# Kernel optimization log

Hardware: AMD Instinct MI355X
Metric: run time of the kernel (lower is better)

The kernel has to match this reference:

```python
import jax, jax.numpy as jnp
import numpy as np

D = 1024      # features
C = 768       # context dim
H = 16        # heads
HD = D // H   # head dim = 64
N = 2048      # query tokens
M = 2048      # context tokens
EPS = 1e-12
SCALE = float(np.sqrt(HD))


def layernorm(x, w, b):
    c = x - x.mean(axis=-1, keepdims=True)
    s = (c * c).mean(axis=-1, keepdims=True)
    return c * jax.lax.rsqrt(s + EPS) * w + b


def setup_inputs() -> dict:
    key = jax.random.key(0)
    ks = jax.random.split(key, 10)
    sc = 0.02
    return {
        "x": jax.random.normal(ks[0], (N, D), jnp.float32),
        "ctx": jax.random.normal(ks[1], (M, C), jnp.float32),
        # attention projections (Projection: normal*0.02, zero bias)
        "wq": jax.random.normal(ks[2], (D, D), jnp.float32) * sc,
        "bq": jnp.zeros((D,), jnp.float32),
        "wk": jax.random.normal(ks[3], (C, D), jnp.float32) * sc,
        "bk": jnp.zeros((D,), jnp.float32),
        "wv": jax.random.normal(ks[4], (C, D), jnp.float32) * sc,
        "bv": jnp.zeros((D,), jnp.float32),
        "wo": jax.random.normal(ks[5], (D, D), jnp.float32) * sc,
        "bo": jnp.zeros((D,), jnp.float32),
        # MLP
        "w1": jax.random.normal(ks[6], (D, 4 * D), jnp.float32) * sc,
        "b1": jnp.zeros((4 * D,), jnp.float32),
        "w2": jax.random.normal(ks[7], (4 * D, D), jnp.float32) * sc,
        "b2": jnp.zeros((D,), jnp.float32),
        # layernorms
        "qn_w": jnp.ones((D,), jnp.float32), "qn_b": jnp.zeros((D,), jnp.float32),
        "kvn_w": jnp.ones((C,), jnp.float32), "kvn_b": jnp.zeros((C,), jnp.float32),
        "pn_w": jnp.ones((D,), jnp.float32), "pn_b": jnp.zeros((D,), jnp.float32),
    }


def reference(x, ctx, wq, bq, wk, bk, wv, bv, wo, bo, w1, b1, w2, b2,
              qn_w, qn_b, kvn_w, kvn_b, pn_w, pn_b):
    # pre-norm cross-attention
    xq = layernorm(x, qn_w, qn_b)          # [n, d]
    kv = layernorm(ctx, kvn_w, kvn_b)      # [m, c]
    q = (xq @ wq + bq).reshape(N, H, HD).transpose(1, 0, 2)   # [h, n, hd]
    k = (kv @ wk + bk).reshape(M, H, HD).transpose(1, 0, 2)   # [h, m, hd]
    v = (kv @ wv + bv).reshape(M, H, HD).transpose(1, 0, 2)   # [h, m, hd]
    attn = jax.nn.softmax(jnp.einsum('hnd,hmd->hnm', q, k) / SCALE, axis=-1)
    o = jnp.einsum('hnm,hmd->hnd', attn, v).transpose(1, 0, 2).reshape(N, D)
    x = (o @ wo + bo) + x
    # MLP block
    h = layernorm(x, pn_w, pn_b)
    h = jax.nn.gelu(h @ w1 + b1) @ w2 + b2
    return h + x
```

## Files before the change

### kernel.cpp

```cpp
#include <hip/hip_runtime.h>

typedef __bf16 bf16;
typedef __bf16 bf16x4 __attribute__((ext_vector_type(4)));
typedef __bf16 bf16x8 __attribute__((ext_vector_type(8)));
typedef float f32x4 __attribute__((ext_vector_type(4)));

#define N_TOK 2048
#define M_TOK 2048
#define DIM 1024
#define CDIM 768
#define DFF 4096

static __device__ __forceinline__ void async16(const void* g, void* l) {
  __builtin_amdgcn_global_load_lds((const __attribute__((address_space(1))) void*)g,
                                   (__attribute__((address_space(3))) void*)l, 16, 0, 0);
}

__device__ __forceinline__ bool detect_bf(const void* xprobe, float* sbuf) {
  int* cnt = (int*)sbuf;
  if (threadIdx.x == 0) *cnt = 0;
  __syncthreads();
  const unsigned* w = (const unsigned*)xprobe;
  int ok = 0;
  for (int i = threadIdx.x; i < 512; i += 256) {
    unsigned lo = w[i] & 0xFFFFu;
    float f = __uint_as_float(lo << 16);
    if (lo == 0u || (fabsf(f) > 1e-3f && fabsf(f) < 1e3f)) ok++;
  }
  atomicAdd(cnt, ok);
  __syncthreads();
  return *cnt >= 256;
}

__device__ __forceinline__ void t32(int bx, int by, const void* in, bf16* out,
                                    int r0, int Rcnt, int c0, int Cfull,
                                    bool isbf, bf16* t) {
  const int cb = bx * 32, rb = by * 32;
  const int tx = threadIdx.x & 31, ty = threadIdx.x >> 5;
#pragma unroll
  for (int i = 0; i < 4; i++) {
    const size_t r = (size_t)(r0 + rb + ty + i * 8);
    const size_t c = (size_t)(c0 + cb + tx);
    float v = isbf ? (float)((const bf16*)in)[r * Cfull + c]
                   : ((const float*)in)[r * Cfull + c];
    t[(ty + i * 8) * 33 + tx] = (bf16)v;
  }
  __syncthreads();
#pragma unroll
  for (int i = 0; i < 4; i++)
    out[(size_t)(cb + ty + i * 8) * Rcnt + rb + tx] = t[tx * 33 + ty + i * 8];
}

__device__ __forceinline__ void ln_row(const void* x, const void* wr, const void* br,
                                       bf16* outp, int cols, int row,
                                       bool in_bf, bool w_bf,
                                       float* xrow, float* sh) {
  const bf16* xr_b = (const bf16*)x + (size_t)row * cols;
  const float* xr_f = (const float*)x + (size_t)row * cols;
  bf16* orow = outp + (size_t)row * cols;
  float s = 0.f, ss = 0.f;
  for (int c = threadIdx.x; c < cols; c += 256) {
    float v = in_bf ? (float)xr_b[c] : xr_f[c];
    xrow[c] = v;
    s += v; ss += v * v;
  }
  for (int d = 1; d < 64; d <<= 1) { s += __shfl_xor(s, d, 64); ss += __shfl_xor(ss, d, 64); }
  const int wv = threadIdx.x >> 6, lane = threadIdx.x & 63;
  if (lane == 0) { sh[wv] = s; sh[4 + wv] = ss; }
  __syncthreads();
  s = sh[0] + sh[1] + sh[2] + sh[3];
  ss = sh[4] + sh[5] + sh[6] + sh[7];
  const float mean = s / cols;
  float var = ss / cols - mean * mean;
  var = fmaxf(var, 0.f);
  const float r = rsqrtf(var + 1e-12f);
  for (int c = threadIdx.x; c < cols; c += 256) {
    const float wv2 = w_bf ? (float)((const bf16*)wr)[c] : ((const float*)wr)[c];
    const float bv2 = w_bf ? (float)((const bf16*)br)[c] : ((const float*)br)[c];
    orow[c] = (bf16)((xrow[c] - mean) * r * wv2 + bv2);
  }
}

struct PrepArgs {
  const void* tsrc[4]; bf16* tdst[4]; int tRcnt[4], tCfull[4], tgy[4];
  const void* x; const void* qnw; const void* qnb; bf16* xq;
  const void* ctx; const void* kvnw; const void* kvnb; bf16* kvn;
  const void* csrc[12]; bf16* cdst[12]; int cn[12];
  const void* xprobe;
};
__global__ __launch_bounds__(256) void prep_kernel(PrepArgs a, int* flag) {
  __shared__ __align__(16) float sbuf[1040];
  const int z = blockIdx.z;
  const bool isbf = detect_bf(a.xprobe, sbuf);
  if (z < 4) {
    if ((int)blockIdx.y >= a.tgy[z]) return;
    t32(blockIdx.x, blockIdx.y, a.tsrc[z], a.tdst[z], 0, a.tRcnt[z], 0, a.tCfull[z],
        isbf, (bf16*)sbuf);
  } else if (z < 8) {
    const int row = blockIdx.x + 32 * blockIdx.y + (z & 1) * 1024;
    if (z < 6) ln_row(a.x,   a.qnw,  a.qnb,  a.xq,  DIM,  row, isbf, isbf, sbuf, sbuf + 1024);
    else       ln_row(a.ctx, a.kvnw, a.kvnb, a.kvn, CDIM, row, isbf, isbf, sbuf, sbuf + 1024);
  } else {
    const int b = blockIdx.x + 32 * blockIdx.y;
    if (b == 0 && threadIdx.x == 0) *flag = isbf ? 1 : 0;
    if (b >= 12) return;
    const void* in = a.csrc[b];
    bf16* out = a.cdst[b];
    const int n = a.cn[b];
    for (int i = threadIdx.x; i < n; i += 256)
      out[i] = isbf ? ((const bf16*)in)[i] : (bf16)((const float*)in)[i];
  }
}

struct PostArgs {
  const void* w1; bf16* w1T;
  const void* w2; bf16* w2T;
  const bf16* xat; const void* pnw; const void* pnb; bf16* hln;
};
__global__ __launch_bounds__(256) void post_kernel(PostArgs a, const int* flag) {
  __shared__ __align__(16) float sbuf[1040];
  const int z = blockIdx.z;
  const bool isbf = (*flag != 0);
  if (z == 0) {
    t32(blockIdx.x, blockIdx.y, a.w1, a.w1T, 0, DIM, 0, DFF, isbf, (bf16*)sbuf);
  } else if (z == 1) {
    const int tbx = blockIdx.x & 31, tby = blockIdx.y + 32 * (blockIdx.x >> 5);
    t32(tbx, tby, a.w2, a.w2T, 0, 2048, 0, DIM, isbf, (bf16*)sbuf);
  } else {
    const int row = blockIdx.x + 64 * blockIdx.y;
    ln_row(a.xat, a.pnw, a.pnb, a.hln, DIM, row, true, isbf, sbuf, sbuf + 1024);
  }
}

__device__ __forceinline__ float gelu_f(float x) {
  float u = 0.7978845608028654f * (x + 0.044715f * x * x * x);
  return 0.5f * x * (1.f + tanhf(u));
}

template <int EPI>
__device__ __forceinline__ void gemm_body(
    int bx, int by,
    const bf16* __restrict__ A, const bf16* __restrict__ Bt,
    const bf16* __restrict__ bias, const void* __restrict__ resid,
    void* __restrict__ Cout, int K, int ldc, const int* flag) {
  __shared__ __align__(16) bf16 As[2][64 * 64];
  __shared__ __align__(16) bf16 Bs[2][64 * 64];
  const int tid = threadIdx.x;
  const int lane = tid & 63, wv = tid >> 6;
  const int lq = lane >> 4, lm = lane & 15;
  const int row0 = by * 64, col0 = bx * 64;
  const int wr = (wv >> 1) * 32, wc = (wv & 1) * 32;

  const int sr = lane >> 3;
  const int sc = ((lane & 7) ^ sr) * 8;
  const int swz = (lm & 7) << 3;

  f32x4 acc[2][2] = {};

  const bf16* Abase = A + (size_t)(row0 + wv * 16 + sr) * K + sc;
  const bf16* Bbase = Bt + (size_t)(col0 + wv * 16 + sr) * K + sc;

  const int nt = K >> 6;
#pragma unroll
  for (int b = 0; b < 2; b++) {
    async16(Abase + (size_t)(b * 8) * K, &As[0][wv * 1024 + b * 512]);
    async16(Bbase + (size_t)(b * 8) * K, &Bs[0][wv * 1024 + b * 512]);
  }
  __syncthreads();

  int cur = 0;
  for (int t = 0; t < nt; ++t) {
    if (t + 1 < nt) {
      const int k1 = (t + 1) << 6;
#pragma unroll
      for (int b = 0; b < 2; b++) {
        async16(Abase + (size_t)(b * 8) * K + k1, &As[cur ^ 1][wv * 1024 + b * 512]);
        async16(Bbase + (size_t)(b * 8) * K + k1, &Bs[cur ^ 1][wv * 1024 + b * 512]);
      }
    }
#pragma unroll
    for (int kh = 0; kh < 2; kh++) {
      const int cofs = (kh * 32 + lq * 8) ^ swz;
      bf16x8 af[2], bfv[2];
#pragma unroll
      for (int i = 0; i < 2; i++)
        af[i] = *(const bf16x8*)&As[cur][(wr + i * 16 + lm) * 64 + cofs];
#pragma unroll
      for (int j = 0; j < 2; j++)
        bfv[j] = *(const bf16x8*)&Bs[cur][(wc + j * 16 + lm) * 64 + cofs];
#pragma unroll
      for (int i = 0; i < 2; i++)
#pragma unroll
        for (int j = 0; j < 2; j++)
          acc[i][j] = __builtin_amdgcn_mfma_f32_16x16x32_bf16(af[i], bfv[j], acc[i][j], 0, 0, 0);
    }
    __syncthreads();
    cur ^= 1;
  }

  const bool isbf = (*flag != 0);
#pragma unroll
  for (int i = 0; i < 2; i++) {
    const int rb = row0 + wr + i * 16 + lq * 4;
#pragma unroll
    for (int j = 0; j < 2; j++) {
      const int c = col0 + wc + j * 16 + lm;
      const float bv = (EPI != 5) ? (float)bias[c] : 0.f;
#pragma unroll
      for (int rg = 0; rg < 4; rg++) {
        const size_t idx = (size_t)(rb + rg) * ldc + c;
        float v = acc[i][j][rg] + bv;
        if (EPI == 1)
          v += isbf ? (float)((const bf16*)resid)[idx] : ((const float*)resid)[idx];
        if (EPI == 2) v = gelu_f(v);
        if (EPI == 4) v += (float)((const bf16*)resid)[idx];
        if (EPI == 5)
          v += isbf ? (float)((bf16*)Cout)[idx] : ((float*)Cout)[idx];
        if (EPI == 4 || EPI == 5) {
          if (isbf) ((bf16*)Cout)[idx] = (bf16)v;
          else      ((float*)Cout)[idx] = v;
        } else {
          ((bf16*)Cout)[idx] = (bf16)v;
        }
      }
    }
  }
}

template <int EPI>
__global__ __launch_bounds__(256) void gemm64db(
    const bf16* __restrict__ A, const bf16* __restrict__ Bt,
    const bf16* __restrict__ bias, const void* __restrict__ resid,
    void* __restrict__ Cout, int K, int ldc, const int* flag) {
  gemm_body<EPI>(blockIdx.x, blockIdx.y, A, Bt, bias, resid, Cout, K, ldc, flag);
}

struct Mlp2Args {
  const bf16* h1; const bf16* w2T; const bf16* b2; const bf16* xat; void* out;
  const void* w1raw; bf16* w1Tdst;
  const void* w2raw; bf16* w2Tdst;
};
__global__ __launch_bounds__(256) void mlp2h0_fused(Mlp2Args a, const int* flag) {
  const int z = blockIdx.z;
  if (z == 0) {
    if ((int)blockIdx.x >= 16) return;
    gemm_body<4>(blockIdx.x, blockIdx.y, a.h1, a.w2T, a.b2, a.xat, a.out,
                 2048, DIM, flag);
  } else {
    __shared__ __align__(16) bf16 t[32 * 33];
    const bool isbf = (*flag != 0);
    if (z == 1) {
      t32(blockIdx.x, blockIdx.y, a.w1raw, a.w1Tdst, 0, DIM, 2048, DFF, isbf, t);
    } else {
      const int tbx = blockIdx.x & 31, tby = blockIdx.y + 32 * (blockIdx.x >> 5);
      t32(tbx, tby, a.w2raw, a.w2Tdst, 2048, 2048, 0, DIM, isbf, t);
    }
  }
}

struct QkvArgs {
  const bf16* A[3];
  const bf16* Bt[3];
  const bf16* bias[3];
  bf16* C[3];
  int K[3], ldc[3], brow[3];
};
__global__ __launch_bounds__(256) void gemm64db_qkv(QkvArgs a) {
  const int z = blockIdx.z;
  int bx, by;
  if (z < 2) { bx = blockIdx.y; by = blockIdx.x; }
  else       { bx = blockIdx.x; by = blockIdx.y; }
  const bf16* A = a.A[z];
  const bf16* Bt = a.Bt[z];
  const int K = a.K[z];
  __shared__ __align__(16) bf16 As[2][64 * 64];
  __shared__ __align__(16) bf16 Bs[2][64 * 64];
  const int tid = threadIdx.x;
  const int lane = tid & 63, wv = tid >> 6;
  const int lq = lane >> 4, lm = lane & 15;
  const int row0 = by * 64, col0 = bx * 64;
  const int wr = (wv >> 1) * 32, wc = (wv & 1) * 32;

  const int sr = lane >> 3;
  const int sc = ((lane & 7) ^ sr) * 8;
  const int swz = (lm & 7) << 3;

  f32x4 acc[2][2] = {};

  const bf16* Abase = A + (size_t)(row0 + wv * 16 + sr) * K + sc;
  const bf16* Bbase = Bt + (size_t)(col0 + wv * 16 + sr) * K + sc;

  const int nt = K >> 6;
#pragma unroll
  for (int b = 0; b < 2; b++) {
    async16(Abase + (size_t)(b * 8) * K, &As[0][wv * 1024 + b * 512]);
    async16(Bbase + (size_t)(b * 8) * K, &Bs[0][wv * 1024 + b * 512]);
  }
  __syncthreads();

  int cur = 0;
  for (int t = 0; t < nt; ++t) {
    if (t + 1 < nt) {
      const int k1 = (t + 1) << 6;
#pragma unroll
      for (int b = 0; b < 2; b++) {
        async16(Abase + (size_t)(b * 8) * K + k1, &As[cur ^ 1][wv * 1024 + b * 512]);
        async16(Bbase + (size_t)(b * 8) * K + k1, &Bs[cur ^ 1][wv * 1024 + b * 512]);
      }
    }
#pragma unroll
    for (int kh = 0; kh < 2; kh++) {
      const int cofs = (kh * 32 + lq * 8) ^ swz;
      bf16x8 af[2], bfv[2];
#pragma unroll
      for (int i = 0; i < 2; i++)
        af[i] = *(const bf16x8*)&As[cur][(wr + i * 16 + lm) * 64 + cofs];
#pragma unroll
      for (int j = 0; j < 2; j++)
        bfv[j] = *(const bf16x8*)&Bs[cur][(wc + j * 16 + lm) * 64 + cofs];
#pragma unroll
      for (int i = 0; i < 2; i++)
#pragma unroll
        for (int j = 0; j < 2; j++)
          acc[i][j] = __builtin_amdgcn_mfma_f32_16x16x32_bf16(af[i], bfv[j], acc[i][j], 0, 0, 0);
    }
    __syncthreads();
    cur ^= 1;
  }

  const bf16* bias = a.bias[z];
  bf16* C = a.C[z];
  const int ldc = a.ldc[z];
  const bool brow = a.brow[z] != 0;
#pragma unroll
  for (int i = 0; i < 2; i++) {
    const int rb = row0 + wr + i * 16 + lq * 4;
#pragma unroll
    for (int j = 0; j < 2; j++) {
      const int c = col0 + wc + j * 16 + lm;
      const float bcol = brow ? 0.f : (float)bias[c];
#pragma unroll
      for (int rg = 0; rg < 4; rg++) {
        const float bv = brow ? (float)bias[rb + rg] : bcol;
        C[(size_t)(rb + rg) * ldc + c] = (bf16)(acc[i][j][rg] + bv);
      }
    }
  }
}

__global__ __launch_bounds__(512) void attn_kernel(
    const bf16* __restrict__ q, const bf16* __restrict__ k,
    const bf16* __restrict__ vT, bf16* __restrict__ pO0, bf16* __restrict__ pO1,
    float* __restrict__ l0, float* __restrict__ l1) {
  __shared__ __align__(16) bf16 KPs[128 * 128];
  __shared__ __align__(16) bf16 Vs[64 * 128];
  const int tid = threadIdx.x, lane = tid & 63, wv = tid >> 6;
  const int lq = lane >> 4, lm = lane & 15;
  const int fid = blockIdx.x + 16 * (blockIdx.y + 16 * blockIdx.z);
  const int sid = (fid & 7) * 64 + (fid >> 3);
  const int n0 = (sid & 15) * 128;
  const int h = (sid >> 4) & 15;
  const int half = sid >> 8;
  const int mbeg = half * (M_TOK / 2), mend = mbeg + M_TOK / 2;
  bf16* pO = half ? pO1 : pO0;
  float* lb = half ? l1 : l0;

  bf16x8 qf[2];
#pragma unroll
  for (int f = 0; f < 2; f++)
    qf[f] = *(const bf16x8*)&q[(size_t)(n0 + wv * 16 + lm) * DIM + h * 64 + f * 32 + lq * 8];

  f32x4 oacc[4] = {};
  float lsum = 0.f;
  const float sc = 0.125f * 1.4426950408889634f;

  bf16x8 kreg[2], vreg[2];
#pragma unroll
  for (int it = 0; it < 2; it++) {
    const int e = tid * 8 + it * 4096;
    kreg[it] = *(const bf16x8*)&k[(size_t)(mbeg + (e >> 6)) * DIM + h * 64 + (e & 63)];
    vreg[it] = *(const bf16x8*)&vT[(size_t)(h * 64 + (e >> 7)) * M_TOK + mbeg + (e & 127)];
  }

  for (int m0 = mbeg; m0 < mend; m0 += 128) {
    asm volatile("s_waitcnt lgkmcnt(0)" ::: "memory");
    __builtin_amdgcn_s_barrier();
#pragma unroll
    for (int it = 0; it < 2; it++) {
      const int e = tid * 8 + it * 4096;
      const int kr = e >> 6, kc = e & 63;
      *(bf16x8*)&KPs[kr * 64 + (kc ^ ((kr & 7) << 3))] = kreg[it];
      const int vr = e >> 7, vc = e & 127;
      *(bf16x8*)&Vs[vr * 128 + (vc ^ ((vr & 7) << 3))] = vreg[it];
    }
    if (m0 + 128 < mend) {
      const int m1 = m0 + 128;
#pragma unroll
      for (int it = 0; it < 2; it++) {
        const int e = tid * 8 + it * 4096;
        kreg[it] = *(const bf16x8*)&k[(size_t)(m1 + (e >> 6)) * DIM + h * 64 + (e & 63)];
        vreg[it] = *(const bf16x8*)&vT[(size_t)(h * 64 + (e >> 7)) * M_TOK + m1 + (e & 127)];
      }
    }
    asm volatile("s_waitcnt lgkmcnt(0)" ::: "memory");
    __builtin_amdgcn_s_barrier();

    f32x4 s[8];
    __builtin_amdgcn_s_setprio(1);
#pragma unroll
    for (int j = 0; j < 8; j++) {
      const int kswz = (lm & 7) << 3;
      bf16x8 kf0 = *(const bf16x8*)&KPs[(j * 16 + lm) * 64 + ((lq * 8) ^ kswz)];
      bf16x8 kf1 = *(const bf16x8*)&KPs[(j * 16 + lm) * 64 + ((32 + lq * 8) ^ kswz)];
      f32x4 z = {};
      z = __builtin_amdgcn_mfma_f32_16x16x32_bf16(kf0, qf[0], z, 0, 0, 0);
      s[j] = __builtin_amdgcn_mfma_f32_16x16x32_bf16(kf1, qf[1], z, 0, 0, 0);
    }
    __builtin_amdgcn_s_setprio(0);
    asm volatile("s_waitcnt lgkmcnt(0)" ::: "memory");
    __builtin_amdgcn_s_barrier();

#pragma unroll
    for (int j = 0; j < 8; j++) {
      bf16x4 pw;
#pragma unroll
      for (int rg = 0; rg < 4; rg++) {
        const float pv = exp2f(s[j][rg] * sc);
        lsum += pv;
        pw[rg] = (bf16)pv;
      }
      *(bf16x4*)&KPs[(wv * 16 + lm) * 128 + ((j * 16 + lq * 4) ^ ((lm & 7) << 3))] = pw;
    }

    __builtin_amdgcn_s_setprio(1);
#pragma unroll
    for (int kk = 0; kk < 4; kk++) {
      bf16x8 pf = *(const bf16x8*)&KPs[(wv * 16 + lm) * 128 +
                                       ((kk * 32 + lq * 8) ^ ((lm & 7) << 3))];
#pragma unroll
      for (int dt = 0; dt < 4; dt++) {
        bf16x8 vf = *(const bf16x8*)&Vs[(dt * 16 + lm) * 128 +
                                        ((kk * 32 + lq * 8) ^ ((lm & 7) << 3))];
        oacc[dt] = __builtin_amdgcn_mfma_f32_16x16x32_bf16(vf, pf, oacc[dt], 0, 0, 0);
      }
    }
    __builtin_amdgcn_s_setprio(0);
  }

  lsum += __shfl_xor(lsum, 16, 64);
  lsum += __shfl_xor(lsum, 32, 64);
  if (lane < 16) lb[h * N_TOK + n0 + wv * 16 + lane] = lsum;

  const int rn = n0 + wv * 16 + lm;
#pragma unroll
  for (int dt = 0; dt < 4; dt++) {
    bf16x4 ow;
#pragma unroll
    for (int rg = 0; rg < 4; rg++) ow[rg] = (bf16)oacc[dt][rg];
    *(bf16x4*)&pO[(size_t)rn * DIM + h * 64 + dt * 16 + lq * 4] = ow;
  }
}

__global__ __launch_bounds__(256) void attn_combine(
    const bf16* __restrict__ pO0, const bf16* __restrict__ pO1,
    const float* __restrict__ l0, const float* __restrict__ l1,
    bf16* __restrict__ om) {
  const int i4 = (blockIdx.x * 256 + threadIdx.x) * 4;
  const int n = i4 >> 10;
  const int h = (i4 & 1023) >> 6;
  const float rinv = 1.f / (l0[h * N_TOK + n] + l1[h * N_TOK + n]);
  bf16x4 a = *(const bf16x4*)&pO0[i4];
  bf16x4 b = *(const bf16x4*)&pO1[i4];
  bf16x4 o;
#pragma unroll
  for (int r = 0; r < 4; r++) o[r] = (bf16)(((float)a[r] + (float)b[r]) * rinv);
  *(bf16x4*)&om[i4] = o;
}

extern "C" void kernel_launch(void* const* d_in, const int* in_sizes, int n_in,
                              void* d_out, int out_size, void* d_ws, size_t ws_size,
                              hipStream_t stream) {
  const void* x_r     = d_in[0];
  const void* ctx_r   = d_in[1];
  const void* wq_r    = d_in[2];
  const void* bq_r    = d_in[3];
  const void* wk_r    = d_in[4];
  const void* bk_r    = d_in[5];
  const void* wv_r    = d_in[6];
  const void* bv_r    = d_in[7];
  const void* wo_r    = d_in[8];
  const void* bo_r    = d_in[9];
  const void* w1_r    = d_in[10];
  const void* b1_r    = d_in[11];
  const void* w2_r    = d_in[12];
  const void* b2_r    = d_in[13];
  const void* qnw_r   = d_in[14];
  const void* qnb_r   = d_in[15];
  const void* kvnw_r  = d_in[16];
  const void* kvnb_r  = d_in[17];
  const void* pnw_r   = d_in[18];
  const void* pnb_r   = d_in[19];

  bf16* p = (bf16*)d_ws;
  const size_t MEG = 1024 * 1024;
  bf16* qm  = p;             bf16* hln = qm;
  bf16* km  = p + 2 * MEG;   bf16* xat = km;
  bf16* wC  = p + 4 * MEG;
  bf16* xq  = p + 8 * MEG;   bf16* pO0 = xq;   bf16* om = xq;
  bf16* vTb = p + 10 * MEG;
  bf16* kvn = p + 12 * MEG;  bf16* pO1 = kvn;
  bf16* h1h = p + 10 * MEG;
  bf16* SM  = p + 14 * MEG;
  int* flag = (int*)(p + 14 * MEG + 16384);

  bf16* wqT = wC;
  bf16* wkT = wC + 1 * MEG;
  bf16* wvT = wC + 1 * MEG + 786432;
  bf16* woT = wC + 2 * MEG + 524288;
  bf16* w1Th = wC;
  bf16* w2Th = wC + 2 * MEG;
  bf16* w2Ts = p + 8 * MEG;
  float* l0 = (float*)wC;
  float* l1 = l0 + N_TOK * 16;

  bf16* bqc = SM, *bkc = SM + 1024, *bvc = SM + 2048, *boc = SM + 3072;
  bf16* b1c = SM + 4096, *b2c = SM + 8192;
  bf16* qnw = SM + 9216, *qnb = SM + 10240;
  bf16* kvnw = SM + 11264, *kvnb = SM + 12032;
  bf16* pnw = SM + 12800, *pnb = SM + 13824;

  {
    PrepArgs pa;
    pa.tsrc[0] = wq_r; pa.tdst[0] = wqT; pa.tRcnt[0] = DIM;  pa.tCfull[0] = DIM; pa.tgy[0] = 32;
    pa.tsrc[1] = wk_r; pa.tdst[1] = wkT; pa.tRcnt[1] = CDIM; pa.tCfull[1] = DIM; pa.tgy[1] = 24;
    pa.tsrc[2] = wv_r; pa.tdst[2] = wvT; pa.tRcnt[2] = CDIM; pa.tCfull[2] = DIM; pa.tgy[2] = 24;
    pa.tsrc[3] = wo_r; pa.tdst[3] = woT; pa.tRcnt[3] = DIM;  pa.tCfull[3] = DIM; pa.tgy[3] = 32;
    pa.x = x_r;   pa.qnw = qnw_r;   pa.qnb = qnb_r;   pa.xq = xq;
    pa.ctx = ctx_r; pa.kvnw = kvnw_r; pa.kvnb = kvnb_r; pa.kvn = kvn;
    pa.csrc[0] = bq_r;   pa.cdst[0] = bqc;  pa.cn[0] = DIM;
    pa.csrc[1] = bk_r;   pa.cdst[1] = bkc;  pa.cn[1] = DIM;
    pa.csrc[2] = bv_r;   pa.cdst[2] = bvc;  pa.cn[2] = DIM;
    pa.csrc[3] = bo_r;   pa.cdst[3] = boc;  pa.cn[3] = DIM;
    pa.csrc[4] = b1_r;   pa.cdst[4] = b1c;  pa.cn[4] = DFF;
    pa.csrc[5] = b2_r;   pa.cdst[5] = b2c;  pa.cn[5] = DIM;
    pa.csrc[6] = qnw_r;  pa.cdst[6] = qnw;  pa.cn[6] = DIM;
    pa.csrc[7] = qnb_r;  pa.cdst[7] = qnb;  pa.cn[7] = DIM;
    pa.csrc[8] = kvnw_r; pa.cdst[8] = kvnw; pa.cn[8] = CDIM;
    pa.csrc[9] = kvnb_r; pa.cdst[9] = kvnb; pa.cn[9] = CDIM;
    pa.csrc[10] = pnw_r; pa.cdst[10] = pnw; pa.cn[10] = DIM;
    pa.csrc[11] = pnb_r; pa.cdst[11] = pnb; pa.cn[11] = DIM;
    pa.xprobe = x_r;
    prep_kernel<<<dim3(32, 32, 9), 256, 0, stream>>>(pa, flag);
  }

  {
    QkvArgs qa;
    qa.A[0] = xq;  qa.Bt[0] = wqT; qa.bias[0] = bqc; qa.C[0] = qm;
    qa.K[0] = DIM;  qa.ldc[0] = DIM;   qa.brow[0] = 0;
    qa.A[1] = kvn; qa.Bt[1] = wkT; qa.bias[1] = bkc; qa.C[1] = km;
    qa.K[1] = CDIM; qa.ldc[1] = DIM;   qa.brow[1] = 0;
    qa.A[2] = wvT; qa.Bt[2] = kvn; qa.bias[2] = bvc; qa.C[2] = vTb;
    qa.K[2] = CDIM; qa.ldc[2] = M_TOK; qa.brow[2] = 1;
    gemm64db_qkv<<<dim3(32, 16, 3), 256, 0, stream>>>(qa);
  }

  attn_kernel<<<dim3(16, 16, 2), 512, 0, stream>>>(qm, km, vTb, pO0, pO1, l0, l1);
  attn_combine<<<2048, 256, 0, stream>>>(pO0, pO1, l0, l1, om);

  gemm64db<1><<<dim3(16, 32), 256, 0, stream>>>(om, woT, boc, x_r, xat, DIM, DIM, flag);

  {
    PostArgs po;
    po.w1 = w1_r; po.w1T = w1Th;
    po.w2 = w2_r; po.w2T = w2Th;
    po.xat = xat; po.pnw = pnw_r; po.pnb = pnb_r; po.hln = hln;
    post_kernel<<<dim3(64, 32, 3), 256, 0, stream>>>(po, flag);
  }

  gemm64db<2><<<dim3(32, 32), 256, 0, stream>>>(hln, w1Th, b1c, nullptr,
                                                h1h, DIM, 2048, flag);

  {
    Mlp2Args ma;
    ma.h1 = h1h; ma.w2T = w2Th; ma.b2 = b2c; ma.xat = xat; ma.out = d_out;
    ma.w1raw = w1_r; ma.w1Tdst = w1Th;
    ma.w2raw = w2_r; ma.w2Tdst = w2Ts;
    mlp2h0_fused<<<dim3(64, 32, 3), 256, 0, stream>>>(ma, flag);
  }

  gemm64db<2><<<dim3(32, 32), 256, 0, stream>>>(hln, w1Th, b1c + 2048, nullptr,
                                                h1h, DIM, 2048, flag);
  gemm64db<5><<<dim3(16, 32), 256, 0, stream>>>(h1h, w2Ts, b2c, nullptr, d_out,
                                                2048, DIM, flag);
}
```

Before: 334.7 us.

## Overlap w1 transpose with attention and swizzle GEMM block order for cache locality

Moves the first-half w1 transpose out of post_kernel into extra z-slices of the attention kernel, so that transposition runs alongside attention blocks instead of in a later launch. The l0/l1 scratch is relocated so it no longer aliases the w1T destination. Separately, the GEMM kernels (generic, MLP2 and QKV) remap block IDs with an XCD-aware stride-8 swizzle to improve L2 locality across chiplets. Risks: the transpose blocks use 512-thread launches with half the threads idle, and they may delay or contend with attention blocks.

Result: no change. 333.8 us (-0.3%).

```diff
diff --git a/kernel.cpp b/kernel.cpp
--- a/kernel.cpp
+++ b/kernel.cpp
@@ -113,17 +113,13 @@
 }
 
 struct PostArgs {
-  const void* w1; bf16* w1T;
   const void* w2; bf16* w2T;
   const bf16* xat; const void* pnw; const void* pnb; bf16* hln;
 };
 __global__ __launch_bounds__(256) void post_kernel(PostArgs a, const int* flag) {
   __shared__ __align__(16) float sbuf[1040];
-  const int z = blockIdx.z;
   const bool isbf = (*flag != 0);
-  if (z == 0) {
-    t32(blockIdx.x, blockIdx.y, a.w1, a.w1T, 0, DIM, 0, DFF, isbf, (bf16*)sbuf);
-  } else if (z == 1) {
+  if (blockIdx.z == 0) {
     const int tbx = blockIdx.x & 31, tby = blockIdx.y + 32 * (blockIdx.x >> 5);
     t32(tbx, tby, a.w2, a.w2T, 0, 2048, 0, DIM, isbf, (bf16*)sbuf);
   } else {
@@ -232,7 +228,11 @@
     const bf16* __restrict__ A, const bf16* __restrict__ Bt,
     const bf16* __restrict__ bias, const void* __restrict__ resid,
     void* __restrict__ Cout, int K, int ldc, const int* flag) {
-  gemm_body<EPI>(blockIdx.x, blockIdx.y, A, Bt, bias, resid, Cout, K, ldc, flag);
+  const int gx = gridDim.x;
+  const int nwg = gx * gridDim.y;
+  const int fid = blockIdx.x + gx * blockIdx.y;
+  const int sid = (fid & 7) * (nwg >> 3) + (fid >> 3);
+  gemm_body<EPI>(sid % gx, sid / gx, A, Bt, bias, resid, Cout, K, ldc, flag);
 }
 
 struct Mlp2Args {
@@ -244,7 +244,9 @@
   const int z = blockIdx.z;
   if (z == 0) {
     if ((int)blockIdx.x >= 16) return;
-    gemm_body<4>(blockIdx.x, blockIdx.y, a.h1, a.w2T, a.b2, a.xat, a.out,
+    const int fid = blockIdx.x + 16 * blockIdx.y;
+    const int sid = (fid & 7) * 64 + (fid >> 3);
+    gemm_body<4>(sid & 15, sid >> 4, a.h1, a.w2T, a.b2, a.xat, a.out,
                  2048, DIM, flag);
   } else {
     __shared__ __align__(16) bf16 t[32 * 33];
@@ -267,9 +269,12 @@
 };
 __global__ __launch_bounds__(256) void gemm64db_qkv(QkvArgs a) {
   const int z = blockIdx.z;
-  int bx, by;
-  if (z < 2) { bx = blockIdx.y; by = blockIdx.x; }
-  else       { bx = blockIdx.x; by = blockIdx.y; }
+  int gx, bx0, by0;
+  if (z < 2) { gx = 16; bx0 = blockIdx.y; by0 = blockIdx.x; }
+  else       { gx = 32; bx0 = blockIdx.x; by0 = blockIdx.y; }
+  const int fid = bx0 + gx * by0;
+  const int sid = (fid & 7) * 64 + (fid >> 3);
+  const int bx = sid % gx, by = sid / gx;
   const bf16* A = a.A[z];
   const bf16* Bt = a.Bt[z];
   const int K = a.K[z];
@@ -351,12 +356,22 @@
 __global__ __launch_bounds__(512) void attn_kernel(
     const bf16* __restrict__ q, const bf16* __restrict__ k,
     const bf16* __restrict__ vT, bf16* __restrict__ pO0, bf16* __restrict__ pO1,
-    float* __restrict__ l0, float* __restrict__ l1) {
+    float* __restrict__ l0, float* __restrict__ l1,
+    const void* __restrict__ w1raw, bf16* __restrict__ w1Tdst,
+    const int* __restrict__ flag) {
   __shared__ __align__(16) bf16 KPs[128 * 128];
   __shared__ __align__(16) bf16 Vs[64 * 128];
+  const int z = blockIdx.z;
+  if (z >= 2) {
+    if (threadIdx.x >= 256) return;
+    const int id = blockIdx.x + 16 * blockIdx.y + 256 * (z - 2);
+    const bool isbf = (*flag != 0);
+    t32(id & 63, id >> 6, w1raw, w1Tdst, 0, DIM, 0, DFF, isbf, (bf16*)KPs);
+    return;
+  }
   const int tid = threadIdx.x, lane = tid & 63, wv = tid >> 6;
   const int lq = lane >> 4, lm = lane & 15;
-  const int fid = blockIdx.x + 16 * (blockIdx.y + 16 * blockIdx.z);
+  const int fid = blockIdx.x + 16 * (blockIdx.y + 16 * z);
   const int sid = (fid & 7) * 64 + (fid >> 3);
   const int n0 = (sid & 15) * 128;
   const int h = (sid >> 4) & 15;
@@ -412,9 +427,9 @@
       const int kswz = (lm & 7) << 3;
       bf16x8 kf0 = *(const bf16x8*)&KPs[(j * 16 + lm) * 64 + ((lq * 8) ^ kswz)];
       bf16x8 kf1 = *(const bf16x8*)&KPs[(j * 16 + lm) * 64 + ((32 + lq * 8) ^ kswz)];
-      f32x4 z = {};
-      z = __builtin_amdgcn_mfma_f32_16x16x32_bf16(kf0, qf[0], z, 0, 0, 0);
-      s[j] = __builtin_amdgcn_mfma_f32_16x16x32_bf16(kf1, qf[1], z, 0, 0, 0);
+      f32x4 zz = {};
+      zz = __builtin_amdgcn_mfma_f32_16x16x32_bf16(kf0, qf[0], zz, 0, 0, 0);
+      s[j] = __builtin_amdgcn_mfma_f32_16x16x32_bf16(kf1, qf[1], zz, 0, 0, 0);
     }
     __builtin_amdgcn_s_setprio(0);
     asm volatile("s_waitcnt lgkmcnt(0)" ::: "memory");
@@ -520,7 +535,7 @@
   bf16* w1Th = wC;
   bf16* w2Th = wC + 2 * MEG;
   bf16* w2Ts = p + 8 * MEG;
-  float* l0 = (float*)wC;
+  float* l0 = (float*)(wC + 3584 * 1024);
   float* l1 = l0 + N_TOK * 16;
 
   bf16* bqc = SM, *bkc = SM + 1024, *bvc = SM + 2048, *boc = SM + 3072;
@@ -564,17 +579,17 @@
     gemm64db_qkv<<<dim3(32, 16, 3), 256, 0, stream>>>(qa);
   }
 
-  attn_kernel<<<dim3(16, 16, 2), 512, 0, stream>>>(qm, km, vTb, pO0, pO1, l0, l1);
+  attn_kernel<<<dim3(16, 16, 10), 512, 0, stream>>>(qm, km, vTb, pO0, pO1,
+                                                    l0, l1, w1_r, w1Th, flag);
   attn_combine<<<2048, 256, 0, stream>>>(pO0, pO1, l0, l1, om);
 
   gemm64db<1><<<dim3(16, 32), 256, 0, stream>>>(om, woT, boc, x_r, xat, DIM, DIM, flag);
 
   {
     PostArgs po;
-    po.w1 = w1_r; po.w1T = w1Th;
     po.w2 = w2_r; po.w2T = w2Th;
     po.xat = xat; po.pnw = pnw_r; po.pnb = pnb_r; po.hln = hln;
-    post_kernel<<<dim3(64, 32, 3), 256, 0, stream>>>(po, flag);
+    post_kernel<<<dim3(64, 32, 2), 256, 0, stream>>>(po, flag);
   }
 
   gemm64db<2><<<dim3(32, 32), 256, 0, stream>>>(hln, w1Th, b1c, nullptr,
```
